# Optimization experiments

Measured on AMD Instinct MI355X. Metric: run time of the kernel, lower is better.

The kernel has to match this reference:

```python
import jax, jax.numpy as jnp
import numpy as np

T, B, DIM_IN, DIM_STATE, NUM_CLASSES = 256, 64, 256, 512, 10000


def setup_inputs() -> dict:
    key = jax.random.key(0)
    ks = jax.random.split(key, 6)
    inputs = jax.random.normal(ks[0], (T, B, DIM_IN), dtype=jnp.float32)
    labels = jax.random.uniform(ks[1], (T, B, NUM_CLASSES), dtype=jnp.float32)
    labels = labels / jnp.sum(labels, axis=-1, keepdims=True)  # soft label distributions
    initial_state = jnp.zeros((B, DIM_STATE), dtype=jnp.float32)
    initial_output = jnp.zeros((B, DIM_STATE), dtype=jnp.float32)
    # LSTM cell params: gates packed as [i, f, g, o]
    Wx = jax.random.normal(ks[2], (DIM_IN, 4 * DIM_STATE), dtype=jnp.float32) * (1.0 / np.sqrt(DIM_IN))
    Wh = jax.random.normal(ks[3], (DIM_STATE, 4 * DIM_STATE), dtype=jnp.float32) * (1.0 / np.sqrt(DIM_STATE))
    b = jnp.zeros((4 * DIM_STATE,), dtype=jnp.float32)
    # Final FC (softmax head) params
    Wo = jax.random.normal(ks[4], (DIM_STATE, NUM_CLASSES), dtype=jnp.float32) * (1.0 / np.sqrt(DIM_STATE))
    bo = jnp.zeros((NUM_CLASSES,), dtype=jnp.float32)
    return {"inputs": inputs, "labels": labels, "initial_state": initial_state,
            "initial_output": initial_output, "Wx": Wx, "Wh": Wh, "b": b, "Wo": Wo, "bo": bo}


def reference(inputs, labels, initial_state, initial_output, Wx, Wh, b, Wo, bo):
    def step(carry, x_t):
        h, c = carry  # h: [B, DIM_STATE] previous output; c: [B, DIM_STATE] cell state
        z = x_t @ Wx + h @ Wh + b  # [B, 4*DIM_STATE]
        i, f, g, o = jnp.split(z, 4, axis=-1)
        c = jax.nn.sigmoid(f) * c + jax.nn.sigmoid(i) * jnp.tanh(g)
        h = jax.nn.sigmoid(o) * jnp.tanh(c)
        return (h, c), h

    _, hs = jax.lax.scan(step, (initial_output, initial_state), inputs)  # hs: [T, B, DIM_STATE]
    logits = jnp.einsum('tbs,sc->tbc', hs, Wo) + bo  # [T, B, NUM_CLASSES]
    log_p = jax.nn.log_softmax(logits, axis=-1)
    predictions = jnp.exp(log_p)  # softmax probabilities
    # softmax_cross_entropy_with_logits per (t, b), then mean over all
    total_loss = -jnp.mean(jnp.sum(labels * log_p, axis=-1))
    return predictions, total_loss
```

## Files before the change

### kernel.cpp

```cpp
#include <hip/hip_runtime.h>
#include <hip/hip_bf16.h>
#include <math.h>

#define T_STEPS 256
#define BATCH 64
#define DIN 256
#define DSTATE 512
#define NGATE 2048
#define NCLS 10000
#define NCLS_PAD 10112
#define ROWS 16384
#define SCAN_BLOCKS 64
#define GROUP_BLOCKS 16
#define CHUNK_ROWS 4096

typedef __attribute__((ext_vector_type(8))) short bf16x8;
typedef __attribute__((ext_vector_type(4))) float f32x4;

__device__ inline unsigned short f2b(float x) {
    __hip_bfloat16 h = __float2bfloat16(x);
    return *(unsigned short*)&h;
}
__device__ inline float b2f(unsigned short u) {
    return __uint_as_float(((unsigned int)u) << 16);
}


__global__ void init_bar(unsigned* __restrict__ bar) {
    bar[threadIdx.x] = 0u;
}

__global__ void f32_to_bf16(const float* __restrict__ in, unsigned short* __restrict__ out, int n4) {
    int i = blockIdx.x * 256 + threadIdx.x;
    if (i >= n4) return;
    float4 v = *(const float4*)&in[i * 4];
    ushort4 o;
    o.x = f2b(v.x); o.y = f2b(v.y); o.z = f2b(v.z); o.w = f2b(v.w);
    *(ushort4*)&out[i * 4] = o;
}

__global__ void build_wT(const float* __restrict__ W, unsigned short* __restrict__ WT,
                         int kshift, int total) {
    int e = blockIdx.x * 256 + threadIdx.x;
    if (e >= total) return;
    int jp = e >> kshift;
    int k = e & ((1 << kshift) - 1);
    int s = jp >> 2, g = jp & 3;
    WT[e] = f2b(W[(size_t)k * NGATE + g * DSTATE + s]);
}

__global__ void build_bias(const float* __restrict__ b, float* __restrict__ bp) {
    int jp = blockIdx.x * 256 + threadIdx.x;
    if (jp >= NGATE) return;
    bp[jp] = b[(jp & 3) * DSTATE + (jp >> 2)];
}

__launch_bounds__(256)
__global__ void transpose_wo(const float* __restrict__ Wo, unsigned short* __restrict__ WoT) {
    __shared__ float tile[64][65];
    const int tid = threadIdx.x;
    const int n0 = blockIdx.x * 64, k0 = blockIdx.y * 64;
    #pragma unroll
    for (int r = 0; r < 16; ++r) {
        int k = (tid >> 6) + r * 4;
        int n = tid & 63;
        float v = (n0 + n < NCLS) ? Wo[(size_t)(k0 + k) * NCLS + n0 + n] : 0.f;
        tile[k][n] = v;
    }
    __syncthreads();
    #pragma unroll
    for (int r = 0; r < 16; ++r) {
        int n = (tid >> 6) + r * 4;
        int k = tid & 63;
        WoT[(size_t)(n0 + n) * DSTATE + k0 + k] = f2b(tile[k][n]);
    }
}

__launch_bounds__(256)
__global__ void zx_gemm(const unsigned short* __restrict__ Xb,
                        const unsigned short* __restrict__ WxT,
                        const float* __restrict__ bp,
                        unsigned short* __restrict__ ZxT) {
    __shared__ unsigned short As[64][264];
    __shared__ unsigned short Bs[128][264];
    __shared__ float zls[4][32][65];
    const int tid = threadIdx.x;
    const int t = blockIdx.x;
    const int n0 = blockIdx.y * 128;
    const int wave = tid >> 6, lane = tid & 63, mr = lane & 15, g = lane >> 4;

    #pragma unroll
    for (int r = 0; r < 8; ++r) {
        int c = r * 256 + tid; int row = c >> 5, q = c & 31;
        *(int4*)&As[row][q * 8] = *(const int4*)&Xb[((size_t)t * 64 + row) * DIN + q * 8];
    }
    #pragma unroll
    for (int r = 0; r < 16; ++r) {
        int c = r * 256 + tid; int row = c >> 5, q = c & 31;
        *(int4*)&Bs[row][q * 8] = *(const int4*)&WxT[(size_t)(n0 + row) * DIN + q * 8];
    }
    __syncthreads();

    f32x4 acc[4][2] = {};
    #pragma unroll
    for (int kt = 0; kt < DIN; kt += 32) {
        bf16x8 af[4], bf[2];
        #pragma unroll
        for (int fm = 0; fm < 4; ++fm) af[fm] = *(const bf16x8*)&As[fm * 16 + mr][kt + g * 8];
        #pragma unroll
        for (int fn = 0; fn < 2; ++fn) bf[fn] = *(const bf16x8*)&Bs[wave * 32 + fn * 16 + mr][kt + g * 8];
        #pragma unroll
        for (int fm = 0; fm < 4; ++fm)
            #pragma unroll
            for (int fn = 0; fn < 2; ++fn)
                acc[fm][fn] = __builtin_amdgcn_mfma_f32_16x16x32_bf16(af[fm], bf[fn], acc[fm][fn], 0, 0, 0);
    }
    #pragma unroll
    for (int fm = 0; fm < 4; ++fm)
        #pragma unroll
        for (int fn = 0; fn < 2; ++fn)
            #pragma unroll
            for (int r = 0; r < 4; ++r)
                zls[wave][fn * 16 + mr][fm * 16 + g * 4 + r] = acc[fm][fn][r];
    #pragma unroll 4
    for (int jr = 0; jr < 32; ++jr) {
        int j = n0 + wave * 32 + jr;
        float v = zls[wave][jr][lane] + bp[j];
        ZxT[((size_t)t * NGATE + j) * 64 + lane] = f2b(v);
    }
}

__device__ __forceinline__ void groupbar(unsigned* cnt, unsigned* flg, unsigned want, int tid) {
    __syncthreads();
    if (tid == 0) {
        unsigned old = __hip_atomic_fetch_add(cnt, 1u, __ATOMIC_ACQ_REL, __HIP_MEMORY_SCOPE_AGENT);
        if (old == GROUP_BLOCKS - 1) {
            __hip_atomic_store(cnt, 0u, __ATOMIC_RELAXED, __HIP_MEMORY_SCOPE_AGENT);
            __hip_atomic_store(flg, want, __ATOMIC_RELEASE, __HIP_MEMORY_SCOPE_AGENT);
        } else {
            while (__hip_atomic_load(flg, __ATOMIC_RELAXED, __HIP_MEMORY_SCOPE_AGENT) < want) {}
            (void)__hip_atomic_load(flg, __ATOMIC_ACQUIRE, __HIP_MEMORY_SCOPE_AGENT);
        }
    }
    __syncthreads();
}

__launch_bounds__(256, 1)
__global__ void lstm_scan_mfma(const unsigned short* __restrict__ h0b,
                               const float* __restrict__ c0,
                               const unsigned short* __restrict__ WhT,
                               const unsigned short* __restrict__ ZxT,
                               unsigned short* __restrict__ hsb,
                               unsigned* __restrict__ bar) {
    __shared__ unsigned short Wl[128][520];
    __shared__ unsigned short hT[16][520];
    __shared__ float zb[16][132];
    const int tid = threadIdx.x;
    const int bid = blockIdx.x;
    const int grp = bid >> 4;
    const int w   = bid & 15;
    const int b0  = grp * 16;
    const int j0  = w * 128;
    const int s0  = w * 32;
    const int wave = tid >> 6, lane = tid & 63, mr = lane & 15, gl = lane >> 4;
    unsigned* bcnt = bar + grp * 64;
    unsigned* bflg = bar + grp * 64 + 32;

    #pragma unroll 4
    for (int r = 0; r < 32; ++r) {
        int c = r * 256 + tid; int row = c >> 6, q = c & 63;
        *(int4*)&Wl[row][q * 8] = *(const int4*)&WhT[(size_t)(j0 + row) * DSTATE + q * 8];
    }

    const int gb  = lane >> 2;
    const int slg = wave * 8 + (lane & 3) * 2;
    float creg0 = c0[(b0 + gb) * DSTATE + s0 + slg];
    float creg1 = c0[(b0 + gb) * DSTATE + s0 + slg + 1];
    __syncthreads();

    const size_t zo0 = ((size_t)(j0 + wave * 32 + mr)) * 64 + b0 + gl * 4;
    const size_t zo1 = ((size_t)(j0 + wave * 32 + 16 + mr)) * 64 + b0 + gl * 4;
    ushort4 za0 = *(const ushort4*)&ZxT[zo0];
    ushort4 za1 = *(const ushort4*)&ZxT[zo1];

    for (int t = 0; t < T_STEPS; ++t) {
        const unsigned short* hsrc = t ? (hsb + (size_t)(t - 1) * BATCH * DSTATE) : h0b;
        #pragma unroll
        for (int r = 0; r < 4; ++r) {
            int c = r * 256 + tid; int row = c >> 6, q = c & 63;
            *(int4*)&hT[row][q * 8] = *(const int4*)&hsrc[(size_t)(b0 + row) * DSTATE + q * 8];
        }
        __syncthreads();

        f32x4 acc0, acc1;
        acc0[0] = b2f(za0.x); acc0[1] = b2f(za0.y); acc0[2] = b2f(za0.z); acc0[3] = b2f(za0.w);
        acc1[0] = b2f(za1.x); acc1[1] = b2f(za1.y); acc1[2] = b2f(za1.z); acc1[3] = b2f(za1.w);
        if (t + 1 < T_STEPS) {
            za0 = *(const ushort4*)&ZxT[(size_t)(t + 1) * NGATE * 64 + zo0];
            za1 = *(const ushort4*)&ZxT[(size_t)(t + 1) * NGATE * 64 + zo1];
        }
        #pragma unroll
        for (int kt = 0; kt < DSTATE; kt += 32) {
            bf16x8 af = *(const bf16x8*)&hT[mr][kt + gl * 8];
            acc0 = __builtin_amdgcn_mfma_f32_16x16x32_bf16(af, *(const bf16x8*)&Wl[wave * 32 + mr][kt + gl * 8], acc0, 0, 0, 0);
            acc1 = __builtin_amdgcn_mfma_f32_16x16x32_bf16(af, *(const bf16x8*)&Wl[wave * 32 + 16 + mr][kt + gl * 8], acc1, 0, 0, 0);
        }
        #pragma unroll
        for (int r = 0; r < 4; ++r) {
            zb[gl * 4 + r][wave * 32 + mr] = acc0[r];
            zb[gl * 4 + r][wave * 32 + 16 + mr] = acc1[r];
        }
        {
            float zi0 = zb[gb][slg * 4 + 0], zf0 = zb[gb][slg * 4 + 1];
            float zg0 = zb[gb][slg * 4 + 2], zo0v = zb[gb][slg * 4 + 3];
            float zi1 = zb[gb][slg * 4 + 4], zf1 = zb[gb][slg * 4 + 5];
            float zg1 = zb[gb][slg * 4 + 6], zo1v = zb[gb][slg * 4 + 7];
            float i0 = 1.f / (1.f + expf(-zi0)), f0 = 1.f / (1.f + expf(-zf0));
            float o0 = 1.f / (1.f + expf(-zo0v)), g0 = tanhf(zg0);
            float i1 = 1.f / (1.f + expf(-zi1)), f1 = 1.f / (1.f + expf(-zf1));
            float o1 = 1.f / (1.f + expf(-zo1v)), g1 = tanhf(zg1);
            creg0 = f0 * creg0 + i0 * g0;
            creg1 = f1 * creg1 + i1 * g1;
            float h0v = o0 * tanhf(creg0);
            float h1v = o1 * tanhf(creg1);
            ushort2 hv; hv.x = f2b(h0v); hv.y = f2b(h1v);
            *(ushort2*)&hsb[((size_t)t * BATCH + b0 + gb) * DSTATE + s0 + slg] = hv;
        }
        if (t != T_STEPS - 1)
            groupbar(bcnt, bflg, (unsigned)(t + 1), tid);
    }
}

__launch_bounds__(256)
__global__ void gemm_logits_bf16(const unsigned short* __restrict__ A,
                                 const unsigned short* __restrict__ Bt,
                                 const float* __restrict__ bo,
                                 unsigned short* __restrict__ Cb) {
    __shared__ unsigned short As[128 * 32];
    __shared__ unsigned short Bs[128 * 32];
    const int tid = threadIdx.x;
    const int wave = tid >> 6, lane = tid & 63;
    const int wm = wave >> 1, wn = wave & 1;
    const int m0 = blockIdx.y * 128, n0 = blockIdx.x * 128;
    const int g = lane >> 4, mr = lane & 15;

    const int ch0 = wave * 64 + lane;
    const int ch1 = (4 + wave) * 64 + lane;
    const int row0 = ch0 >> 2, q0 = ch0 & 3;
    const int row1 = ch1 >> 2, q1 = ch1 & 3;

    f32x4 acc[4][4] = {};
    for (int kt = 0; kt < DSTATE; kt += 32) {
        __builtin_amdgcn_global_load_lds(
            (const __attribute__((address_space(1))) void*)&A[(size_t)(m0 + row0) * DSTATE + kt + q0 * 8],
            (__attribute__((address_space(3))) void*)&As[ch0 * 8 - lane * 8], 16, 0, 0);
        __builtin_amdgcn_global_load_lds(
            (const __attribute__((address_space(1))) void*)&A[(size_t)(m0 + row1) * DSTATE + kt + q1 * 8],
            (__attribute__((address_space(3))) void*)&As[ch1 * 8 - lane * 8], 16, 0, 0);
        __builtin_amdgcn_global_load_lds(
            (const __attribute__((address_space(1))) void*)&Bt[(size_t)(n0 + row0) * DSTATE + kt + q0 * 8],
            (__attribute__((address_space(3))) void*)&Bs[ch0 * 8 - lane * 8], 16, 0, 0);
        __builtin_amdgcn_global_load_lds(
            (const __attribute__((address_space(1))) void*)&Bt[(size_t)(n0 + row1) * DSTATE + kt + q1 * 8],
            (__attribute__((address_space(3))) void*)&Bs[ch1 * 8 - lane * 8], 16, 0, 0);
        __syncthreads();

        bf16x8 af[4], bf[4];
        #pragma unroll
        for (int f = 0; f < 4; ++f) {
            af[f] = *(const bf16x8*)&As[(wm * 64 + f * 16 + mr) * 32 + g * 8];
            bf[f] = *(const bf16x8*)&Bs[(wn * 64 + f * 16 + mr) * 32 + g * 8];
        }
        #pragma unroll
        for (int fm = 0; fm < 4; ++fm)
            #pragma unroll
            for (int fn = 0; fn < 4; ++fn)
                acc[fm][fn] = __builtin_amdgcn_mfma_f32_16x16x32_bf16(af[fm], bf[fn], acc[fm][fn], 0, 0, 0);
        __syncthreads();
    }
    #pragma unroll
    for (int fm = 0; fm < 4; ++fm) {
        #pragma unroll
        for (int fn = 0; fn < 4; ++fn) {
            int col = n0 + wn * 64 + fn * 16 + mr;
            if (col >= NCLS) continue;
            float bias = bo[col];
            #pragma unroll
            for (int r = 0; r < 4; ++r) {
                int row = m0 + wm * 64 + fm * 16 + g * 4 + r;
                Cb[(size_t)row * NCLS + col] = f2b(acc[fm][fn][r] + bias);
            }
        }
    }
}

__launch_bounds__(256)
__global__ void gemm_logits_mfma(const unsigned short* __restrict__ A,
                                 const unsigned short* __restrict__ Bt,
                                 const float* __restrict__ bo,
                                 float* __restrict__ C) {
    __shared__ unsigned short As[128 * 32];
    __shared__ unsigned short Bs[128 * 32];
    const int tid = threadIdx.x;
    const int wave = tid >> 6, lane = tid & 63;
    const int wm = wave >> 1, wn = wave & 1;
    const int m0 = blockIdx.y * 128, n0 = blockIdx.x * 128;
    const int g = lane >> 4, mr = lane & 15;

    const int ch0 = wave * 64 + lane;
    const int ch1 = (4 + wave) * 64 + lane;
    const int row0 = ch0 >> 2, q0 = ch0 & 3;
    const int row1 = ch1 >> 2, q1 = ch1 & 3;

    f32x4 acc[4][4] = {};
    for (int kt = 0; kt < DSTATE; kt += 32) {
        __builtin_amdgcn_global_load_lds(
            (const __attribute__((address_space(1))) void*)&A[(size_t)(m0 + row0) * DSTATE + kt + q0 * 8],
            (__attribute__((address_space(3))) void*)&As[ch0 * 8 - lane * 8], 16, 0, 0);
        __builtin_amdgcn_global_load_lds(
            (const __attribute__((address_space(1))) void*)&A[(size_t)(m0 + row1) * DSTATE + kt + q1 * 8],
            (__attribute__((address_space(3))) void*)&As[ch1 * 8 - lane * 8], 16, 0, 0);
        __builtin_amdgcn_global_load_lds(
            (const __attribute__((address_space(1))) void*)&Bt[(size_t)(n0 + row0) * DSTATE + kt + q0 * 8],
            (__attribute__((address_space(3))) void*)&Bs[ch0 * 8 - lane * 8], 16, 0, 0);
        __builtin_amdgcn_global_load_lds(
            (const __attribute__((address_space(1))) void*)&Bt[(size_t)(n0 + row1) * DSTATE + kt + q1 * 8],
            (__attribute__((address_space(3))) void*)&Bs[ch1 * 8 - lane * 8], 16, 0, 0);
        __syncthreads();

        bf16x8 af[4], bf[4];
        #pragma unroll
        for (int f = 0; f < 4; ++f) {
            af[f] = *(const bf16x8*)&As[(wm * 64 + f * 16 + mr) * 32 + g * 8];
            bf[f] = *(const bf16x8*)&Bs[(wn * 64 + f * 16 + mr) * 32 + g * 8];
        }
        #pragma unroll
        for (int fm = 0; fm < 4; ++fm)
            #pragma unroll
            for (int fn = 0; fn < 4; ++fn)
                acc[fm][fn] = __builtin_amdgcn_mfma_f32_16x16x32_bf16(af[fm], bf[fn], acc[fm][fn], 0, 0, 0);
        __syncthreads();
    }
    #pragma unroll
    for (int fm = 0; fm < 4; ++fm) {
        #pragma unroll
        for (int fn = 0; fn < 4; ++fn) {
            int col = n0 + wn * 64 + fn * 16 + mr;
            if (col >= NCLS) continue;
            float bias = bo[col];
            #pragma unroll
            for (int r = 0; r < 4; ++r) {
                int row = m0 + wm * 64 + fm * 16 + g * 4 + r;
                C[(size_t)row * NCLS + col] = acc[fm][fn][r] + bias;
            }
        }
    }
}

__device__ inline float wave_reduce_max(float v) {
    #pragma unroll
    for (int off = 32; off > 0; off >>= 1) v = fmaxf(v, __shfl_xor(v, off));
    return v;
}
__device__ inline float wave_reduce_sum(float v) {
    #pragma unroll
    for (int off = 32; off > 0; off >>= 1) v += __shfl_xor(v, off);
    return v;
}

__launch_bounds__(256)
__global__ void softmax_loss_bf16(const unsigned short* __restrict__ Cb,
                                  const float* __restrict__ labels,
                                  float* __restrict__ probs,
                                  float* __restrict__ rowloss) {
    __shared__ float row[NCLS];
    __shared__ float sm[4];
    const int tid = threadIdx.x;
    const size_t base = (size_t)blockIdx.x * NCLS;

    float m = -INFINITY;
    for (int c8 = tid; c8 < NCLS / 8; c8 += 256) {
        ushort4 u0 = *(const ushort4*)&Cb[base + c8 * 8];
        ushort4 u1 = *(const ushort4*)&Cb[base + c8 * 8 + 4];
        float v0 = b2f(u0.x), v1 = b2f(u0.y), v2 = b2f(u0.z), v3 = b2f(u0.w);
        float v4 = b2f(u1.x), v5 = b2f(u1.y), v6 = b2f(u1.z), v7 = b2f(u1.w);
        float4 a = {v0, v1, v2, v3}, b = {v4, v5, v6, v7};
        *(float4*)&row[c8 * 8] = a;
        *(float4*)&row[c8 * 8 + 4] = b;
        m = fmaxf(m, fmaxf(fmaxf(fmaxf(v0, v1), fmaxf(v2, v3)),
                           fmaxf(fmaxf(v4, v5), fmaxf(v6, v7))));
    }
    m = wave_reduce_max(m);
    if ((tid & 63) == 0) sm[tid >> 6] = m;
    __syncthreads();
    m = fmaxf(fmaxf(sm[0], sm[1]), fmaxf(sm[2], sm[3]));
    __syncthreads();

    float s = 0.f, dot = 0.f;
    for (int c4 = tid; c4 < NCLS / 4; c4 += 256) {
        float4 v = *(const float4*)&row[c4 * 4];
        float4 lb = *(const float4*)&labels[base + c4 * 4];
        s += expf(v.x - m) + expf(v.y - m) + expf(v.z - m) + expf(v.w - m);
        dot += lb.x * v.x + lb.y * v.y + lb.z * v.z + lb.w * v.w;
    }
    s = wave_reduce_sum(s);
    if ((tid & 63) == 0) sm[tid >> 6] = s;
    __syncthreads();
    s = sm[0] + sm[1] + sm[2] + sm[3];
    __syncthreads();
    dot = wave_reduce_sum(dot);
    if ((tid & 63) == 0) sm[tid >> 6] = dot;
    __syncthreads();
    dot = sm[0] + sm[1] + sm[2] + sm[3];

    float inv = 1.f / s;
    for (int c4 = tid; c4 < NCLS / 4; c4 += 256) {
        float4 v = *(const float4*)&row[c4 * 4];
        float4 o;
        o.x = expf(v.x - m) * inv; o.y = expf(v.y - m) * inv;
        o.z = expf(v.z - m) * inv; o.w = expf(v.w - m) * inv;
        *(float4*)&probs[base + c4 * 4] = o;
    }
    if (tid == 0) rowloss[blockIdx.x] = (m + logf(s)) - dot;
}

__launch_bounds__(256)
__global__ void softmax_loss(float* __restrict__ logits,
                             const float* __restrict__ labels,
                             float* __restrict__ rowloss) {
    __shared__ float row[NCLS];
    __shared__ float sm[4];
    const int tid = threadIdx.x;
    const size_t base = (size_t)blockIdx.x * NCLS;

    float m = -INFINITY;
    for (int c4 = tid; c4 < NCLS / 4; c4 += 256) {
        float4 v = *(const float4*)&logits[base + c4 * 4];
        *(float4*)&row[c4 * 4] = v;
        m = fmaxf(fmaxf(m, fmaxf(v.x, v.y)), fmaxf(v.z, v.w));
    }
    m = wave_reduce_max(m);
    if ((tid & 63) == 0) sm[tid >> 6] = m;
    __syncthreads();
    m = fmaxf(fmaxf(sm[0], sm[1]), fmaxf(sm[2], sm[3]));
    __syncthreads();

    float s = 0.f, dot = 0.f;
    for (int c4 = tid; c4 < NCLS / 4; c4 += 256) {
        float4 v = *(const float4*)&row[c4 * 4];
        float4 lb = *(const float4*)&labels[base + c4 * 4];
        s += expf(v.x - m) + expf(v.y - m) + expf(v.z - m) + expf(v.w - m);
        dot += lb.x * v.x + lb.y * v.y + lb.z * v.z + lb.w * v.w;
    }
    s = wave_reduce_sum(s);
    if ((tid & 63) == 0) sm[tid >> 6] = s;
    __syncthreads();
    s = sm[0] + sm[1] + sm[2] + sm[3];
    __syncthreads();
    dot = wave_reduce_sum(dot);
    if ((tid & 63) == 0) sm[tid >> 6] = dot;
    __syncthreads();
    dot = sm[0] + sm[1] + sm[2] + sm[3];

    float inv = 1.f / s;
    for (int c4 = tid; c4 < NCLS / 4; c4 += 256) {
        float4 v = *(const float4*)&row[c4 * 4];
        float4 o;
        o.x = expf(v.x - m) * inv; o.y = expf(v.y - m) * inv;
        o.z = expf(v.z - m) * inv; o.w = expf(v.w - m) * inv;
        *(float4*)&logits[base + c4 * 4] = o;
    }
    if (tid == 0) rowloss[blockIdx.x] = (m + logf(s)) - dot;
}

__launch_bounds__(256)
__global__ void loss_reduce(const float* __restrict__ rowloss, float* __restrict__ out) {
    __shared__ float sm[4];
    float s = 0.f;
    for (int i = threadIdx.x; i < ROWS; i += 256) s += rowloss[i];
    s = wave_reduce_sum(s);
    if ((threadIdx.x & 63) == 0) sm[threadIdx.x >> 6] = s;
    __syncthreads();
    if (threadIdx.x == 0) out[0] = (sm[0] + sm[1] + sm[2] + sm[3]) * (1.f / ROWS);
}

extern "C" void kernel_launch(void* const* d_in, const int* in_sizes, int n_in,
                              void* d_out, int out_size, void* d_ws, size_t ws_size,
                              hipStream_t stream) {
    const float* inputs = (const float*)d_in[0];
    const float* labels = (const float*)d_in[1];
    const float* c0     = (const float*)d_in[2];
    const float* h0     = (const float*)d_in[3];
    const float* Wx     = (const float*)d_in[4];
    const float* Wh     = (const float*)d_in[5];
    const float* bias   = (const float*)d_in[6];
    const float* Wo     = (const float*)d_in[7];
    const float* bo     = (const float*)d_in[8];
    float* out = (float*)d_out;

    float* ws = (float*)d_ws;
    float* bp       = ws;
    float* rowloss  = bp + 2048;
    unsigned short* WhT = (unsigned short*)(rowloss + 16384);
    unsigned short* WxT = WhT + 1048576;
    unsigned short* Xb  = WxT + 524288;
    unsigned short* h0b = Xb + 4194304;
    unsigned short* hsb = h0b + 32768;
    unsigned short* WoT = hsb + 8388608;
    unsigned short* ZxT = WoT + 5177344;
    unsigned* bar = (unsigned*)(ZxT + 33554432);
    unsigned short* Cb = (unsigned short*)(bar + 256);

    size_t base_bytes = (size_t)((char*)Cb - (char*)d_ws);
    size_t need_bf16 = base_bytes + (size_t)CHUNK_ROWS * NCLS * sizeof(unsigned short);
    bool use_bf16 = (ws_size >= need_bf16);

    init_bar<<<1, 256, 0, stream>>>(bar);
    f32_to_bf16<<<(ROWS * DIN / 4 + 255) / 256, 256, 0, stream>>>(inputs, Xb, ROWS * DIN / 4);
    f32_to_bf16<<<(BATCH * DSTATE / 4 + 255) / 256, 256, 0, stream>>>(h0, h0b, BATCH * DSTATE / 4);
    build_wT<<<(NGATE * DSTATE + 255) / 256, 256, 0, stream>>>(Wh, WhT, 9, NGATE * DSTATE);
    build_wT<<<(NGATE * DIN + 255) / 256, 256, 0, stream>>>(Wx, WxT, 8, NGATE * DIN);
    build_bias<<<(NGATE + 255) / 256, 256, 0, stream>>>(bias, bp);
    transpose_wo<<<dim3(NCLS_PAD / 64, DSTATE / 64), 256, 0, stream>>>(Wo, WoT);

    zx_gemm<<<dim3(T_STEPS, NGATE / 128), 256, 0, stream>>>(Xb, WxT, bp, ZxT);

    void* args[] = {(void*)&h0b, (void*)&c0, (void*)&WhT, (void*)&ZxT, (void*)&hsb, (void*)&bar};
    hipLaunchCooperativeKernel((const void*)lstm_scan_mfma, dim3(SCAN_BLOCKS), dim3(256),
                               args, 0, stream);

    if (use_bf16) {
        for (int row0 = 0; row0 < ROWS; row0 += CHUNK_ROWS) {
            gemm_logits_bf16<<<dim3(NCLS_PAD / 128, CHUNK_ROWS / 128), 256, 0, stream>>>(
                hsb + (size_t)row0 * DSTATE, WoT, bo, Cb);
            softmax_loss_bf16<<<CHUNK_ROWS, 256, 0, stream>>>(
                Cb, labels + (size_t)row0 * NCLS, out + (size_t)row0 * NCLS, rowloss + row0);
        }
    } else {
        gemm_logits_mfma<<<dim3(NCLS_PAD / 128, ROWS / 128), 256, 0, stream>>>(hsb, WoT, bo, out);
        softmax_loss<<<ROWS, 256, 0, stream>>>(out, labels, rowloss);
    }
    loss_reduce<<<1, 256, 0, stream>>>(rowloss, out + (size_t)ROWS * NCLS);
}
```

Baseline: 2.009 ms.

## Merge prep kernels, swizzle logits GEMM grid, fuse label dot into GEMM epilogue

Replaces seven small preprocessing launches with one combined prep kernel that dispatches on block index. The logits GEMM now uses a 1D grid with an XCD-style swizzle of tile order, and its epilogue computes partial label-logit dot products per column slot. Those partials go to a small workspace that the softmax kernel sums, so softmax no longer reads labels. The epilogue now does uncoalesced label reads and extra shuffles, and it needs a bit more workspace.

```diff
diff --git a/kernel.cpp b/kernel.cpp
--- a/kernel.cpp
+++ b/kernel.cpp
@@ -13,6 +13,8 @@
 #define SCAN_BLOCKS 64
 #define GROUP_BLOCKS 16
 #define CHUNK_ROWS 4096
+#define NSLOT 158
+#define NSLOT_PAD 160
 
 typedef __attribute__((ext_vector_type(8))) short bf16x8;
 typedef __attribute__((ext_vector_type(4))) float f32x4;
@@ -25,54 +27,59 @@
     return __uint_as_float(((unsigned int)u) << 16);
 }
 
-
-__global__ void init_bar(unsigned* __restrict__ bar) {
-    bar[threadIdx.x] = 0u;
-}
-
-__global__ void f32_to_bf16(const float* __restrict__ in, unsigned short* __restrict__ out, int n4) {
-    int i = blockIdx.x * 256 + threadIdx.x;
-    if (i >= n4) return;
-    float4 v = *(const float4*)&in[i * 4];
-    ushort4 o;
-    o.x = f2b(v.x); o.y = f2b(v.y); o.z = f2b(v.z); o.w = f2b(v.w);
-    *(ushort4*)&out[i * 4] = o;
-}
-
-__global__ void build_wT(const float* __restrict__ W, unsigned short* __restrict__ WT,
-                         int kshift, int total) {
-    int e = blockIdx.x * 256 + threadIdx.x;
-    if (e >= total) return;
-    int jp = e >> kshift;
-    int k = e & ((1 << kshift) - 1);
-    int s = jp >> 2, g = jp & 3;
-    WT[e] = f2b(W[(size_t)k * NGATE + g * DSTATE + s]);
-}
-
-__global__ void build_bias(const float* __restrict__ b, float* __restrict__ bp) {
-    int jp = blockIdx.x * 256 + threadIdx.x;
-    if (jp >= NGATE) return;
-    bp[jp] = b[(jp & 3) * DSTATE + (jp >> 2)];
-}
-
-__launch_bounds__(256)
-__global__ void transpose_wo(const float* __restrict__ Wo, unsigned short* __restrict__ WoT) {
+__launch_bounds__(256)
+__global__ void prep_all(const float* __restrict__ inputs, const float* __restrict__ Wx,
+                         const float* __restrict__ Wh, const float* __restrict__ bias,
+                         const float* __restrict__ h0, const float* __restrict__ Wo,
+                         unsigned short* __restrict__ Xb, unsigned short* __restrict__ WxT,
+                         unsigned short* __restrict__ WhT, float* __restrict__ bp,
+                         unsigned short* __restrict__ h0b, unsigned* __restrict__ bar,
+                         unsigned short* __restrict__ WoT) {
     __shared__ float tile[64][65];
-    const int tid = threadIdx.x;
-    const int n0 = blockIdx.x * 64, k0 = blockIdx.y * 64;
-    #pragma unroll
-    for (int r = 0; r < 16; ++r) {
-        int k = (tid >> 6) + r * 4;
-        int n = tid & 63;
-        float v = (n0 + n < NCLS) ? Wo[(size_t)(k0 + k) * NCLS + n0 + n] : 0.f;
-        tile[k][n] = v;
-    }
-    __syncthreads();
-    #pragma unroll
-    for (int r = 0; r < 16; ++r) {
-        int n = (tid >> 6) + r * 4;
-        int k = tid & 63;
-        WoT[(size_t)(n0 + n) * DSTATE + k0 + k] = f2b(tile[k][n]);
+    const int bid = blockIdx.x;
+    const int tid = threadIdx.x;
+    if (bid < 4096) {
+        int i = bid * 256 + tid;
+        float4 v = *(const float4*)&inputs[(size_t)i * 4];
+        ushort4 o; o.x = f2b(v.x); o.y = f2b(v.y); o.z = f2b(v.z); o.w = f2b(v.w);
+        *(ushort4*)&Xb[(size_t)i * 4] = o;
+    } else if (bid < 8192) {
+        int e = (bid - 4096) * 256 + tid;
+        int jp = e >> 9, k = e & 511;
+        int s = jp >> 2, g = jp & 3;
+        WhT[e] = f2b(Wh[(size_t)k * NGATE + g * DSTATE + s]);
+    } else if (bid < 10240) {
+        int e = (bid - 8192) * 256 + tid;
+        int jp = e >> 8, k = e & 255;
+        int s = jp >> 2, g = jp & 3;
+        WxT[e] = f2b(Wx[(size_t)k * NGATE + g * DSTATE + s]);
+    } else if (bid < 10248) {
+        int jp = (bid - 10240) * 256 + tid;
+        bp[jp] = bias[(jp & 3) * DSTATE + (jp >> 2)];
+    } else if (bid < 10280) {
+        int i = (bid - 10248) * 256 + tid;
+        float4 v = *(const float4*)&h0[(size_t)i * 4];
+        ushort4 o; o.x = f2b(v.x); o.y = f2b(v.y); o.z = f2b(v.z); o.w = f2b(v.w);
+        *(ushort4*)&h0b[(size_t)i * 4] = o;
+    } else if (bid < 10281) {
+        bar[tid] = 0u;
+    } else {
+        int nb = bid - 10281;
+        int n0 = (nb % 158) * 64, k0 = (nb / 158) * 64;
+        #pragma unroll
+        for (int r = 0; r < 16; ++r) {
+            int k = (tid >> 6) + r * 4;
+            int n = tid & 63;
+            float v = (n0 + n < NCLS) ? Wo[(size_t)(k0 + k) * NCLS + n0 + n] : 0.f;
+            tile[k][n] = v;
+        }
+        __syncthreads();
+        #pragma unroll
+        for (int r = 0; r < 16; ++r) {
+            int n = (tid >> 6) + r * 4;
+            int k = tid & 63;
+            WoT[(size_t)(n0 + n) * DSTATE + k0 + k] = f2b(tile[k][n]);
+        }
     }
 }
 
@@ -235,13 +242,18 @@
 __global__ void gemm_logits_bf16(const unsigned short* __restrict__ A,
                                  const unsigned short* __restrict__ Bt,
                                  const float* __restrict__ bo,
-                                 unsigned short* __restrict__ Cb) {
+                                 const float* __restrict__ labels,
+                                 unsigned short* __restrict__ Cb,
+                                 float* __restrict__ dotp) {
     __shared__ unsigned short As[128 * 32];
     __shared__ unsigned short Bs[128 * 32];
     const int tid = threadIdx.x;
     const int wave = tid >> 6, lane = tid & 63;
     const int wm = wave >> 1, wn = wave & 1;
-    const int m0 = blockIdx.y * 128, n0 = blockIdx.x * 128;
+    const int id = blockIdx.x;
+    const int swz = (id & 7) * 316 + (id >> 3);
+    const int m0 = (swz & 31) * 128;
+    const int n0 = (swz >> 5) * 128;
     const int g = lane >> 4, mr = lane & 15;
 
     const int ch0 = wave * 64 + lane;
@@ -280,15 +292,29 @@
     }
     #pragma unroll
     for (int fm = 0; fm < 4; ++fm) {
+        float dots[4] = {0.f, 0.f, 0.f, 0.f};
         #pragma unroll
         for (int fn = 0; fn < 4; ++fn) {
             int col = n0 + wn * 64 + fn * 16 + mr;
-            if (col >= NCLS) continue;
-            float bias = bo[col];
-            #pragma unroll
-            for (int r = 0; r < 4; ++r) {
+            if (col < NCLS) {
+                float bias = bo[col];
+                #pragma unroll
+                for (int r = 0; r < 4; ++r) {
+                    int row = m0 + wm * 64 + fm * 16 + g * 4 + r;
+                    float lg = acc[fm][fn][r] + bias;
+                    Cb[(size_t)row * NCLS + col] = f2b(lg);
+                    dots[r] += labels[(size_t)row * NCLS + col] * lg;
+                }
+            }
+        }
+        #pragma unroll
+        for (int r = 0; r < 4; ++r) {
+            float d = dots[r];
+            d += __shfl_xor(d, 1); d += __shfl_xor(d, 2);
+            d += __shfl_xor(d, 4); d += __shfl_xor(d, 8);
+            if (mr == 0) {
                 int row = m0 + wm * 64 + fm * 16 + g * 4 + r;
-                Cb[(size_t)row * NCLS + col] = f2b(acc[fm][fn][r] + bias);
+                dotp[(size_t)row * NSLOT_PAD + (swz >> 5) * 2 + wn] = d;
             }
         }
     }
@@ -370,7 +396,7 @@
 
 __launch_bounds__(256)
 __global__ void softmax_loss_bf16(const unsigned short* __restrict__ Cb,
-                                  const float* __restrict__ labels,
+                                  const float* __restrict__ dotp,
                                   float* __restrict__ probs,
                                   float* __restrict__ rowloss) {
     __shared__ float row[NCLS];
@@ -396,12 +422,11 @@
     m = fmaxf(fmaxf(sm[0], sm[1]), fmaxf(sm[2], sm[3]));
     __syncthreads();
 
-    float s = 0.f, dot = 0.f;
+    float s = 0.f;
+    float dot = (tid < NSLOT) ? dotp[(size_t)blockIdx.x * NSLOT_PAD + tid] : 0.f;
     for (int c4 = tid; c4 < NCLS / 4; c4 += 256) {
         float4 v = *(const float4*)&row[c4 * 4];
-        float4 lb = *(const float4*)&labels[base + c4 * 4];
         s += expf(v.x - m) + expf(v.y - m) + expf(v.z - m) + expf(v.w - m);
-        dot += lb.x * v.x + lb.y * v.y + lb.z * v.z + lb.w * v.w;
     }
     s = wave_reduce_sum(s);
     if ((tid & 63) == 0) sm[tid >> 6] = s;
@@ -510,18 +535,14 @@
     unsigned short* ZxT = WoT + 5177344;
     unsigned* bar = (unsigned*)(ZxT + 33554432);
     unsigned short* Cb = (unsigned short*)(bar + 256);
-
-    size_t base_bytes = (size_t)((char*)Cb - (char*)d_ws);
-    size_t need_bf16 = base_bytes + (size_t)CHUNK_ROWS * NCLS * sizeof(unsigned short);
+    float* dotp = (float*)(Cb + (size_t)CHUNK_ROWS * NCLS);
+
+    size_t base_bytes = (size_t)((char*)dotp - (char*)d_ws);
+    size_t need_bf16 = base_bytes + (size_t)CHUNK_ROWS * NSLOT_PAD * sizeof(float);
     bool use_bf16 = (ws_size >= need_bf16);
 
-    init_bar<<<1, 256, 0, stream>>>(bar);
-    f32_to_bf16<<<(ROWS * DIN / 4 + 255) / 256, 256, 0, stream>>>(inputs, Xb, ROWS * DIN / 4);
-    f32_to_bf16<<<(BATCH * DSTATE / 4 + 255) / 256, 256, 0, stream>>>(h0, h0b, BATCH * DSTATE / 4);
-    build_wT<<<(NGATE * DSTATE + 255) / 256, 256, 0, stream>>>(Wh, WhT, 9, NGATE * DSTATE);
-    build_wT<<<(NGATE * DIN + 255) / 256, 256, 0, stream>>>(Wx, WxT, 8, NGATE * DIN);
-    build_bias<<<(NGATE + 255) / 256, 256, 0, stream>>>(bias, bp);
-    transpose_wo<<<dim3(NCLS_PAD / 64, DSTATE / 64), 256, 0, stream>>>(Wo, WoT);
+    prep_all<<<11545, 256, 0, stream>>>(inputs, Wx, Wh, bias, h0, Wo,
+                                        Xb, WxT, WhT, bp, h0b, bar, WoT);
 
     zx_gemm<<<dim3(T_STEPS, NGATE / 128), 256, 0, stream>>>(Xb, WxT, bp, ZxT);
 
@@ -531,10 +552,11 @@
 
     if (use_bf16) {
         for (int row0 = 0; row0 < ROWS; row0 += CHUNK_ROWS) {
-            gemm_logits_bf16<<<dim3(NCLS_PAD / 128, CHUNK_ROWS / 128), 256, 0, stream>>>(
-                hsb + (size_t)row0 * DSTATE, WoT, bo, Cb);
+            gemm_logits_bf16<<<2528, 256, 0, stream>>>(
+                hsb + (size_t)row0 * DSTATE, WoT, bo,
+                labels + (size_t)row0 * NCLS, Cb, dotp);
             softmax_loss_bf16<<<CHUNK_ROWS, 256, 0, stream>>>(
-                Cb, labels + (size_t)row0 * NCLS, out + (size_t)row0 * NCLS, rowloss + row0);
+                Cb, dotp, out + (size_t)row0 * NCLS, rowloss + row0);
         }
     } else {
         gemm_logits_mfma<<<dim3(NCLS_PAD / 128, ROWS / 128), 256, 0, stream>>>(hsb, WoT, bo, out);
```

Measured after the change: 2.095 ms. +4.3%, slower.
